# Kernel tuning notes

Measured on AMD Instinct MI355X. Metric: run time of the kernel, lower is better.

The kernel has to match this reference:

```python
import jax, jax.numpy as jnp
import numpy as np
import math

N_NODES = 100000
D = 64
N_EDGES = 1280000
LN_EPS = 1e-5


def setup_inputs() -> dict:
    key = jax.random.key(0)
    ks = jax.random.split(key, 8)
    x = jax.random.normal(ks[0], (N_NODES, D), dtype=jnp.float32)
    edge_index = jax.random.randint(ks[1], (2, N_EDGES), 0, N_NODES, dtype=jnp.int64)
    # xavier_uniform with gain=0.1 for weight matrices
    limit = 0.1 * math.sqrt(6.0 / (D + D))
    qk_w = jax.random.uniform(ks[2], (D, D), dtype=jnp.float32, minval=-limit, maxval=limit)
    v_w = jax.random.uniform(ks[3], (D, D), dtype=jnp.float32, minval=-limit, maxval=limit)
    o_w = jax.random.uniform(ks[4], (D, D), dtype=jnp.float32, minval=-limit, maxval=limit)
    qk_b = jnp.zeros((D,), dtype=jnp.float32)
    v_b = jnp.zeros((D,), dtype=jnp.float32)
    o_b = jnp.zeros((D,), dtype=jnp.float32)
    ln_g = jnp.ones((D,), dtype=jnp.float32)
    ln_b = jnp.zeros((D,), dtype=jnp.float32)
    return {"x": x, "edge_index": edge_index, "qk_w": qk_w, "qk_b": qk_b,
            "v_w": v_w, "v_b": v_b, "o_w": o_w, "o_b": o_b,
            "ln_g": ln_g, "ln_b": ln_b}


def reference(x, edge_index, qk_w, qk_b, v_w, v_b, o_w, o_b, ln_g, ln_b):
    n = x.shape[0]
    # shared Q/K projection and V projection (torch Linear: x @ W^T + b)
    qk = x @ qk_w.T + qk_b            # [N, D]
    v = x @ v_w.T + v_b               # [N, D]

    src = edge_index[0]
    dst = edge_index[1]

    # edge-wise attention logits: <q[dst], k[src]> / sqrt(D), clamped
    scores = jnp.sum(qk[dst] * qk[src], axis=-1) / math.sqrt(v.shape[-1])  # [E]
    scores = jnp.clip(scores, -5.0, 5.0)

    # segment softmax over incoming edges of each destination node
    seg_max = jax.ops.segment_max(scores, dst, num_segments=n)   # [N], -inf for empty
    e = jnp.exp(scores - seg_max[dst])                           # [E]
    seg_sum = jax.ops.segment_sum(e, dst, num_segments=n)        # [N]
    attn = e / seg_sum[dst]                                      # [E]

    # weighted scatter-add aggregation (nodes with no in-edges stay zero)
    out = jax.ops.segment_sum(attn[:, None] * v[src], dst, num_segments=n)  # [N, D]

    out = out @ o_w.T + o_b

    # LayerNorm(out + residual)
    h = out + x
    mu = jnp.mean(h, axis=-1, keepdims=True)
    var = jnp.mean(jnp.square(h - mu), axis=-1, keepdims=True)
    h = (h - mu) * jax.lax.rsqrt(var + LN_EPS)
    return h * ln_g + ln_b
```

## Files before the change

### kernel.cpp

```cpp
#include <hip/hip_runtime.h>
#include <hip/hip_bf16.h>
#include <math.h>

#define DD 64
#define CAP 64
#define BINSZ 256
#define EPB 2048
#define NBINS 391
#define LN_EPS 1e-5f

typedef float v2f __attribute__((ext_vector_type(2)));
typedef __attribute__((ext_vector_type(8))) short bf16x8;
typedef __attribute__((ext_vector_type(4))) float f32x4;

__device__ __forceinline__ float bf2f(unsigned short u) {
    return __uint_as_float(((unsigned)u) << 16);
}
__device__ __forceinline__ short f2bf(float f) {
    __hip_bfloat16 h = __float2bfloat16(f);
    return *reinterpret_cast<short*>(&h);
}
__device__ __forceinline__ bf16x8 cvt8(const float* p) {
    float4 a = *(const float4*)p;
    float4 b = *(const float4*)(p + 4);
    bf16x8 r;
    r[0] = f2bf(a.x); r[1] = f2bf(a.y); r[2] = f2bf(a.z); r[3] = f2bf(a.w);
    r[4] = f2bf(b.x); r[5] = f2bf(b.y); r[6] = f2bf(b.z); r[7] = f2bf(b.w);
    return r;
}
__device__ __forceinline__ unsigned char f2fp8(float f) {
    return (unsigned char)(__builtin_amdgcn_cvt_pk_fp8_f32(f, 0.f, 0, false) & 0xff);
}

struct PartSh { int lhist[512]; int loff[512]; int wsum[16]; unsigned lstage[EPB]; };
struct ProjSh { unsigned char lkv[64 * 128]; unsigned short lq[64 * 64]; };

__global__ __launch_bounds__(256) void prep_kernel(
    const float* __restrict__ x,
    const float* __restrict__ qk_w, const float* __restrict__ qk_b,
    const float* __restrict__ v_w,  const float* __restrict__ v_b,
    const int* __restrict__ eidx, int2* __restrict__ cotab,
    unsigned* __restrict__ ebuf,
    __hip_bfloat16* __restrict__ qk, unsigned char* __restrict__ kv,
    int n, int E, int AB)
{
    __shared__ union { PartSh p; ProjSh j; } sh;

    int bid = blockIdx.x;
    int tid = threadIdx.x;
    if (bid < AB) {
        for (int b = tid; b < 512; b += 256) sh.p.lhist[b] = 0;
        __syncthreads();
        int nv = E >> 2;
        const uint4* dst4 = (const uint4*)(eidx + E);
        const uint4* src4 = (const uint4*)(eidx);
        uint4 d[2], s[2];
        int rnk[8];
        bool ok[2];
        #pragma unroll
        for (int g = 0; g < 2; ++g) {
            int i4 = bid * 512 + tid + g * 256;
            ok[g] = i4 < nv;
            if (ok[g]) {
                d[g] = dst4[i4];
                s[g] = src4[i4];
                #pragma unroll
                for (int c = 0; c < 4; ++c) {
                    unsigned dd = (c == 0) ? d[g].x : (c == 1) ? d[g].y
                                : (c == 2) ? d[g].z : d[g].w;
                    rnk[g * 4 + c] = atomicAdd(&sh.p.lhist[dd >> 8], 1);
                }
            }
        }
        __syncthreads();
        int lane = tid & 63, wv = tid >> 6;
        int c0 = sh.p.lhist[2 * tid];
        int c1 = sh.p.lhist[2 * tid + 1];
        int pair = c0 + c1;
        int val = pair;
        #pragma unroll
        for (int st = 1; st < 64; st <<= 1) {
            int t = __shfl_up(val, st);
            if (lane >= st) val += t;
        }
        if (lane == 63) sh.p.wsum[wv] = val;
        __syncthreads();
        int wpre = 0;
        #pragma unroll
        for (int w = 0; w < 4; ++w) wpre += (w < wv) ? sh.p.wsum[w] : 0;
        int excl = val + wpre - pair;
        sh.p.loff[2 * tid]     = excl;
        sh.p.loff[2 * tid + 1] = excl + c0;
        __syncthreads();
        #pragma unroll
        for (int g = 0; g < 2; ++g) {
            if (ok[g]) {
                #pragma unroll
                for (int c = 0; c < 4; ++c) {
                    unsigned dd = (c == 0) ? d[g].x : (c == 1) ? d[g].y
                                : (c == 2) ? d[g].z : d[g].w;
                    unsigned ss = (c == 0) ? s[g].x : (c == 1) ? s[g].y
                                : (c == 2) ? s[g].z : s[g].w;
                    int bin = dd >> 8;
                    sh.p.lstage[sh.p.loff[bin] + rnk[g * 4 + c]] = (ss << 8) | (dd & 255);
                }
            }
        }
        __syncthreads();
        unsigned* myebuf = ebuf + (size_t)bid * EPB;
        for (int e = tid; e < EPB; e += 256) myebuf[e] = sh.p.lstage[e];
        int2* myco = cotab + (size_t)bid * NBINS;
        for (int b = tid; b < NBINS; b += 256)
            myco[b] = make_int2(sh.p.lhist[b], sh.p.loff[b]);
    } else {
        int pbid = bid - AB;
        int wave = tid >> 6, lane = tid & 63;
        int node0 = pbid * 64 + wave * 16;
        int lr = lane & 15;
        int lk = (lane >> 4) << 3;

        if (node0 < n) {
            int arow = min(node0 + lr, n - 1);
            const float* xr = x + (size_t)arow * 64 + lk;
            bf16x8 A0 = cvt8(xr);
            bf16x8 A1 = cvt8(xr + 32);

            float qbias[4] = {qk_b[lr], qk_b[16 + lr], qk_b[32 + lr], qk_b[48 + lr]};
            float vbias[4] = {v_b[lr],  v_b[16 + lr],  v_b[32 + lr],  v_b[48 + lr]};

            f32x4 z = {0.f, 0.f, 0.f, 0.f};
            f32x4 accq[4], accv[4];
            #pragma unroll
            for (int ct = 0; ct < 4; ++ct) {
                const float* wq = qk_w + (size_t)(ct * 16 + lr) * 64 + lk;
                bf16x8 Bq0 = cvt8(wq);
                bf16x8 Bq1 = cvt8(wq + 32);
                f32x4 aq = __builtin_amdgcn_mfma_f32_16x16x32_bf16(A0, Bq0, z, 0, 0, 0);
                aq = __builtin_amdgcn_mfma_f32_16x16x32_bf16(A1, Bq1, aq, 0, 0, 0);
                accq[ct] = aq;
                const float* wv2 = v_w + (size_t)(ct * 16 + lr) * 64 + lk;
                bf16x8 Bv0 = cvt8(wv2);
                bf16x8 Bv1 = cvt8(wv2 + 32);
                f32x4 av = __builtin_amdgcn_mfma_f32_16x16x32_bf16(A0, Bv0, z, 0, 0, 0);
                av = __builtin_amdgcn_mfma_f32_16x16x32_bf16(A1, Bv1, av, 0, 0, 0);
                accv[ct] = av;
            }
            #pragma unroll
            for (int ct = 0; ct < 4; ++ct) {
                int dim  = ct * 16 + lr;
                int koff = ((dim >> 2) << 3) + (dim & 3);
                #pragma unroll
                for (int r = 0; r < 4; ++r) {
                    int ndl = wave * 16 + ((lane >> 4) << 2) + r;
                    float q = accq[ct][r] + qbias[ct];
                    float v = accv[ct][r] + vbias[ct];
                    sh.j.lq[ndl * 64 + dim] = (unsigned short)f2bf(q);
                    sh.j.lkv[ndl * 128 + koff]     = f2fp8(q);
                    sh.j.lkv[ndl * 128 + koff + 4] = f2fp8(v);
                }
            }
        }
        __syncthreads();
        int row = tid >> 2;
        size_t gnode = (size_t)pbid * 64 + row;
        if (gnode < (size_t)n) {
            const uint4* skv = (const uint4*)(sh.j.lkv + tid * 32);
            uint4* dkv = (uint4*)(kv + (size_t)pbid * 64 * 128 + tid * 32);
            dkv[0] = skv[0];
            dkv[1] = skv[1];
            const uint4* sq = (const uint4*)((const unsigned char*)sh.j.lq + tid * 32);
            uint4* dq = (uint4*)((unsigned char*)qk + (size_t)pbid * 64 * 128 + tid * 32);
            dq[0] = sq[0];
            dq[1] = sq[1];
        }
    }
}

__global__ __launch_bounds__(512) void bucket_kernel(
    const int2* __restrict__ cotab, const unsigned* __restrict__ ebuf,
    int* __restrict__ deg, int* __restrict__ bucket, int n, int NPB)
{
    __shared__ int lbkt[BINSZ * CAP];
    __shared__ int ldeg[BINSZ];
    int bin = blockIdx.x, tid = threadIdx.x;
    if (tid < BINSZ) ldeg[tid] = 0;
    __syncthreads();
    for (int c = tid; c < NPB; c += 512) {
        int2 co = cotab[(size_t)c * NBINS + bin];
        const unsigned* run = ebuf + (size_t)c * EPB + co.y;
        for (int r = 0; r < co.x; ++r) {
            unsigned e = run[r];
            int rel = e & 255;
            int rr = atomicAdd(&ldeg[rel], 1);
            if (rr < CAP) lbkt[(rel << 6) + rr] = (int)(e >> 8);
        }
    }
    __syncthreads();
    size_t gbase = (size_t)(bin << 8) << 6;
    int node0 = bin << 8;
    const uint4* src = (const uint4*)lbkt;
    uint4* dst = (uint4*)(bucket + gbase);
    for (int i = tid; i < BINSZ * CAP / 4; i += 512) {
        if (node0 + (i >> 4) < n) dst[i] = src[i];
    }
    if (tid < BINSZ) {
        int node = node0 + tid;
        if (node < n) deg[node] = min(ldeg[tid], CAP);
    }
}

__global__ __launch_bounds__(256) void attn_kernel(
    const __hip_bfloat16* __restrict__ qk, const unsigned char* __restrict__ kv,
    const int* __restrict__ deg, const int* __restrict__ bucket,
    __hip_bfloat16* __restrict__ outd, int n)
{
    int tid = threadIdx.x;
    int wave = tid >> 6, lane = tid & 63;
    int node = blockIdx.x * 4 + wave;
    if (node >= n) return;

    int sub = lane >> 4;
    int sl  = lane & 15;

    ushort4 qu = *(const ushort4*)(qk + ((size_t)node << 6) + (sl << 2));
    v2f qlo = {bf2f(qu.x), bf2f(qu.y)};
    v2f qhi = {bf2f(qu.z), bf2f(qu.w)};
    int dn = deg[node];
    int medge = bucket[((size_t)node << 6) + lane];

    float s = 0.f;
    v2f acclo = {0.f, 0.f};
    v2f acchi = {0.f, 0.f};
    const float ESCALE = 0.18033688f;

    for (int base = 0; base < dn; base += 16) {
        int m1 = dn - 1;
        int i0 = base + sub;
        int i1 = i0 + 4, i2 = i0 + 8, i3 = i0 + 12;
        int s0 = __shfl(medge, min(i0, m1));
        int s1 = __shfl(medge, min(i1, m1));
        int s2 = __shfl(medge, min(i2, m1));
        int s3 = __shfl(medge, min(i3, m1));
        uint2 w0 = *(const uint2*)(kv + ((unsigned)s0 << 7) + (sl << 3));
        uint2 w1 = *(const uint2*)(kv + ((unsigned)s1 << 7) + (sl << 3));
        uint2 w2 = *(const uint2*)(kv + ((unsigned)s2 << 7) + (sl << 3));
        uint2 w3 = *(const uint2*)(kv + ((unsigned)s3 << 7) + (sl << 3));
        v2f t0 = qlo * __builtin_amdgcn_cvt_pk_f32_fp8(w0.x, false)
               + qhi * __builtin_amdgcn_cvt_pk_f32_fp8(w0.x, true);
        v2f t1 = qlo * __builtin_amdgcn_cvt_pk_f32_fp8(w1.x, false)
               + qhi * __builtin_amdgcn_cvt_pk_f32_fp8(w1.x, true);
        v2f t2 = qlo * __builtin_amdgcn_cvt_pk_f32_fp8(w2.x, false)
               + qhi * __builtin_amdgcn_cvt_pk_f32_fp8(w2.x, true);
        v2f t3 = qlo * __builtin_amdgcn_cvt_pk_f32_fp8(w3.x, false)
               + qhi * __builtin_amdgcn_cvt_pk_f32_fp8(w3.x, true);
        float p0 = t0.x + t0.y;
        float p1 = t1.x + t1.y;
        float p2 = t2.x + t2.y;
        float p3 = t3.x + t3.y;
        #pragma unroll
        for (int w = 1; w <= 8; w <<= 1) {
            p0 += __shfl_xor(p0, w); p1 += __shfl_xor(p1, w);
            p2 += __shfl_xor(p2, w); p3 += __shfl_xor(p3, w);
        }
        float pe0 = (i0 < dn) ? __builtin_amdgcn_exp2f(p0 * ESCALE) : 0.f;
        float pe1 = (i1 < dn) ? __builtin_amdgcn_exp2f(p1 * ESCALE) : 0.f;
        float pe2 = (i2 < dn) ? __builtin_amdgcn_exp2f(p2 * ESCALE) : 0.f;
        float pe3 = (i3 < dn) ? __builtin_amdgcn_exp2f(p3 * ESCALE) : 0.f;
        s += (pe0 + pe1) + (pe2 + pe3);
        acclo += __builtin_amdgcn_cvt_pk_f32_fp8(w0.y, false) * pe0;
        acchi += __builtin_amdgcn_cvt_pk_f32_fp8(w0.y, true)  * pe0;
        acclo += __builtin_amdgcn_cvt_pk_f32_fp8(w1.y, false) * pe1;
        acchi += __builtin_amdgcn_cvt_pk_f32_fp8(w1.y, true)  * pe1;
        acclo += __builtin_amdgcn_cvt_pk_f32_fp8(w2.y, false) * pe2;
        acchi += __builtin_amdgcn_cvt_pk_f32_fp8(w2.y, true)  * pe2;
        acclo += __builtin_amdgcn_cvt_pk_f32_fp8(w3.y, false) * pe3;
        acchi += __builtin_amdgcn_cvt_pk_f32_fp8(w3.y, true)  * pe3;
    }

    float a0 = acclo.x, a1 = acclo.y, a2 = acchi.x, a3 = acchi.y;
    s  += __shfl_xor(s, 16);  s  += __shfl_xor(s, 32);
    a0 += __shfl_xor(a0, 16); a0 += __shfl_xor(a0, 32);
    a1 += __shfl_xor(a1, 16); a1 += __shfl_xor(a1, 32);
    a2 += __shfl_xor(a2, 16); a2 += __shfl_xor(a2, 32);
    a3 += __shfl_xor(a3, 16); a3 += __shfl_xor(a3, 32);

    float inv = (dn > 0) ? (1.0f / s) : 0.f;
    if (sub == 0) {
        ushort4 o;
        o.x = (unsigned short)f2bf(a0 * inv);
        o.y = (unsigned short)f2bf(a1 * inv);
        o.z = (unsigned short)f2bf(a2 * inv);
        o.w = (unsigned short)f2bf(a3 * inv);
        *(ushort4*)(outd + ((size_t)node << 6) + (sl << 2)) = o;
    }
}

__global__ __launch_bounds__(256) void epi_kernel(
    const __hip_bfloat16* __restrict__ outd, const float* __restrict__ x,
    const float* __restrict__ o_w, const float* __restrict__ o_b,
    const float* __restrict__ ln_g, const float* __restrict__ ln_b,
    float* __restrict__ out, int n)
{
    int tid = threadIdx.x;
    int wave = tid >> 6, lane = tid & 63;
    int node0 = blockIdx.x * 64 + wave * 16;
    if (node0 >= n) return;

    int lr = lane & 15;
    int lk = (lane >> 4) << 3;

    int arow = min(node0 + lr, n - 1);
    const __hip_bfloat16* odr = outd + (size_t)arow * 64 + lk;
    bf16x8 A0 = *(const bf16x8*)odr;
    bf16x8 A1 = *(const bf16x8*)(odr + 32);

    f32x4 z = {0.f, 0.f, 0.f, 0.f};
    f32x4 acc[4];
    #pragma unroll
    for (int ct = 0; ct < 4; ++ct) {
        const float* wo = o_w + (size_t)(ct * 16 + lr) * 64 + lk;
        bf16x8 B0 = cvt8(wo);
        bf16x8 B1 = cvt8(wo + 32);
        f32x4 a = __builtin_amdgcn_mfma_f32_16x16x32_bf16(A0, B0, z, 0, 0, 0);
        a = __builtin_amdgcn_mfma_f32_16x16x32_bf16(A1, B1, a, 0, 0, 0);
        acc[ct] = a;
    }
    float ob[4] = {o_b[lr], o_b[16 + lr], o_b[32 + lr], o_b[48 + lr]};
    float lg[4] = {ln_g[lr], ln_g[16 + lr], ln_g[32 + lr], ln_g[48 + lr]};
    float lb[4] = {ln_b[lr], ln_b[16 + lr], ln_b[32 + lr], ln_b[48 + lr]};

    #pragma unroll
    for (int r = 0; r < 4; ++r) {
        int nd = node0 + ((lane >> 4) << 2) + r;
        if (nd >= n) break;
        float h[4];
        #pragma unroll
        for (int ct = 0; ct < 4; ++ct)
            h[ct] = acc[ct][r] + ob[ct] + x[(size_t)nd * 64 + ct * 16 + lr];
        float m = (h[0] + h[1]) + (h[2] + h[3]);
        #pragma unroll
        for (int w = 1; w <= 8; w <<= 1) m += __shfl_xor(m, w);
        m *= (1.f / 64.f);
        float d0 = h[0] - m, d1 = h[1] - m, d2 = h[2] - m, d3 = h[3] - m;
        float vv = (d0 * d0 + d1 * d1) + (d2 * d2 + d3 * d3);
        #pragma unroll
        for (int w = 1; w <= 8; w <<= 1) vv += __shfl_xor(vv, w);
        vv *= (1.f / 64.f);
        float rs = rsqrtf(vv + LN_EPS);
        float* op = out + (size_t)nd * 64 + lr;
        op[0]  = d0 * rs * lg[0] + lb[0];
        op[16] = d1 * rs * lg[1] + lb[1];
        op[32] = d2 * rs * lg[2] + lb[2];
        op[48] = d3 * rs * lg[3] + lb[3];
    }
}

extern "C" void kernel_launch(void* const* d_in, const int* in_sizes, int n_in,
                              void* d_out, int out_size, void* d_ws, size_t ws_size,
                              hipStream_t stream)
{
    const float* x    = (const float*)d_in[0];
    const int*   eidx = (const int*)  d_in[1];
    const float* qk_w = (const float*)d_in[2];
    const float* qk_b = (const float*)d_in[3];
    const float* v_w  = (const float*)d_in[4];
    const float* v_b  = (const float*)d_in[5];
    const float* o_w  = (const float*)d_in[6];
    const float* o_b  = (const float*)d_in[7];
    const float* ln_g = (const float*)d_in[8];
    const float* ln_b = (const float*)d_in[9];

    const int n = in_sizes[0] / DD;
    const int E = in_sizes[1] / 2;
    const int AB = (E + EPB - 1) / EPB;
    const int PB = (n + 63) / 64;

    char* ws = (char*)d_ws;
    size_t off = 0;
    __hip_bfloat16* qk = (__hip_bfloat16*)(ws + off); off += (size_t)n * 64 * 2;
    unsigned char* kv  = (unsigned char*)(ws + off); off += (size_t)n * 128;
    int* deg    = (int*)(ws + off); off += (size_t)n * 4;
    int* bucket = (int*)(ws + off); off += (size_t)n * CAP * 4;
    int2* cotab = (int2*)(ws + off); off += (size_t)AB * NBINS * 8;
    unsigned* ebuf = (unsigned*)(ws + off); off += (size_t)AB * EPB * 4;
    __hip_bfloat16* outd = (__hip_bfloat16*)(ws + off); off += (size_t)n * 64 * 2;

    prep_kernel<<<AB + PB, 256, 0, stream>>>(x, qk_w, qk_b, v_w, v_b,
                                             eidx, cotab, ebuf, qk, kv, n, E, AB);
    bucket_kernel<<<NBINS, 512, 0, stream>>>(cotab, ebuf, deg, bucket, n, AB);
    attn_kernel<<<(n + 3) / 4, 256, 0, stream>>>(qk, kv, deg, bucket, outd, n);
    epi_kernel<<<(n + 63) / 64, 256, 0, stream>>>(outd, x, o_w, o_b, ln_g, ln_b,
                                                  (float*)d_out, n);
}
```

Measured before the change: 120.7 us.

## Process two destination nodes per wave in attention kernel

Each 64-lane wave now handles two nodes, one per 32-lane half, instead of one. Each half splits into two 16-lane groups that each take four consecutive edges per iteration. The change targets idle lanes on low-degree nodes (average degree about 12.8), where the old 16-edge stride wasted much of the wave. The cost is more shuffles per iteration to fetch edge indices from two registers, plus divergent trip counts between the two halves.

```diff
diff --git a/kernel.cpp b/kernel.cpp
--- a/kernel.cpp
+++ b/kernel.cpp
@@ -216,31 +216,45 @@
 {
     int tid = threadIdx.x;
     int wave = tid >> 6, lane = tid & 63;
-    int node = blockIdx.x * 4 + wave;
-    if (node >= n) return;
-
-    int sub = lane >> 4;
-    int sl  = lane & 15;
-
-    ushort4 qu = *(const ushort4*)(qk + ((size_t)node << 6) + (sl << 2));
+    int half = lane >> 5;
+    int hl   = lane & 31;
+    int sh   = (lane >> 4) & 1;
+    int sl   = lane & 15;
+    int hb   = half << 5;
+
+    int node = blockIdx.x * 8 + wave * 2 + half;
+    bool valid = node < n;
+    int nc = valid ? node : (n - 1);
+
+    ushort4 qu = *(const ushort4*)(qk + ((size_t)nc << 6) + (sl << 2));
     v2f qlo = {bf2f(qu.x), bf2f(qu.y)};
     v2f qhi = {bf2f(qu.z), bf2f(qu.w)};
-    int dn = deg[node];
-    int medge = bucket[((size_t)node << 6) + lane];
+    int dn = valid ? deg[nc] : 0;
+    int medge  = bucket[((size_t)nc << 6) + hl];
+    int medge2 = bucket[((size_t)nc << 6) + 32 + hl];
 
     float s = 0.f;
     v2f acclo = {0.f, 0.f};
     v2f acchi = {0.f, 0.f};
     const float ESCALE = 0.18033688f;
 
-    for (int base = 0; base < dn; base += 16) {
+    for (int base = 0; base < dn; base += 8) {
         int m1 = dn - 1;
-        int i0 = base + sub;
-        int i1 = i0 + 4, i2 = i0 + 8, i3 = i0 + 12;
-        int s0 = __shfl(medge, min(i0, m1));
-        int s1 = __shfl(medge, min(i1, m1));
-        int s2 = __shfl(medge, min(i2, m1));
-        int s3 = __shfl(medge, min(i3, m1));
+        int i0 = base + (sh << 2);
+        int i1 = i0 + 1, i2 = i0 + 2, i3 = i0 + 3;
+        int c0 = min(i0, m1), c1 = min(i1, m1), c2 = min(i2, m1), c3 = min(i3, m1);
+        int u0 = __shfl(medge,  hb | (c0 & 31));
+        int v0_ = __shfl(medge2, hb | (c0 & 31));
+        int u1 = __shfl(medge,  hb | (c1 & 31));
+        int v1_ = __shfl(medge2, hb | (c1 & 31));
+        int u2 = __shfl(medge,  hb | (c2 & 31));
+        int v2_ = __shfl(medge2, hb | (c2 & 31));
+        int u3 = __shfl(medge,  hb | (c3 & 31));
+        int v3_ = __shfl(medge2, hb | (c3 & 31));
+        int s0 = (c0 < 32) ? u0 : v0_;
+        int s1 = (c1 < 32) ? u1 : v1_;
+        int s2 = (c2 < 32) ? u2 : v2_;
+        int s3 = (c3 < 32) ? u3 : v3_;
         uint2 w0 = *(const uint2*)(kv + ((unsigned)s0 << 7) + (sl << 3));
         uint2 w1 = *(const uint2*)(kv + ((unsigned)s1 << 7) + (sl << 3));
         uint2 w2 = *(const uint2*)(kv + ((unsigned)s2 << 7) + (sl << 3));
@@ -278,14 +292,14 @@
     }
 
     float a0 = acclo.x, a1 = acclo.y, a2 = acchi.x, a3 = acchi.y;
-    s  += __shfl_xor(s, 16);  s  += __shfl_xor(s, 32);
-    a0 += __shfl_xor(a0, 16); a0 += __shfl_xor(a0, 32);
-    a1 += __shfl_xor(a1, 16); a1 += __shfl_xor(a1, 32);
-    a2 += __shfl_xor(a2, 16); a2 += __shfl_xor(a2, 32);
-    a3 += __shfl_xor(a3, 16); a3 += __shfl_xor(a3, 32);
+    s  += __shfl_xor(s, 16);
+    a0 += __shfl_xor(a0, 16);
+    a1 += __shfl_xor(a1, 16);
+    a2 += __shfl_xor(a2, 16);
+    a3 += __shfl_xor(a3, 16);
 
     float inv = (dn > 0) ? (1.0f / s) : 0.f;
-    if (sub == 0) {
+    if (sh == 0 && valid) {
         ushort4 o;
         o.x = (unsigned short)f2bf(a0 * inv);
         o.y = (unsigned short)f2bf(a1 * inv);
@@ -388,7 +402,7 @@
     prep_kernel<<<AB + PB, 256, 0, stream>>>(x, qk_w, qk_b, v_w, v_b,
                                              eidx, cotab, ebuf, qk, kv, n, E, AB);
     bucket_kernel<<<NBINS, 512, 0, stream>>>(cotab, ebuf, deg, bucket, n, AB);
-    attn_kernel<<<(n + 3) / 4, 256, 0, stream>>>(qk, kv, deg, bucket, outd, n);
+    attn_kernel<<<(n + 7) / 8, 256, 0, stream>>>(qk, kv, deg, bucket, outd, n);
     epi_kernel<<<(n + 63) / 64, 256, 0, stream>>>(outd, x, o_w, o_b, ln_g, ln_b,
                                                   (float*)d_out, n);
 }
```

Measured after the change: 116.7 us, median of 2. 1.03x faster.
